# Performance work log

Hardware: AMD Instinct MI355X
Metric: run time of the kernel (lower is better)

Reference implementation:

```python
import jax, jax.numpy as jnp
import numpy as np
import math

B, T, NX, H, D = 4, 1024, 1024, 16, 64
KMAX = 32          # rel_kmax
RELV = 64          # rel_vocab_size (tree relation vocab)
NLOC = 64          # local-relation table size
SQRT = 2.0         # args.sqrt
INF = 10000000000.0


def setup_inputs() -> dict:
    key = jax.random.key(0)
    ks = jax.random.split(key, 13)
    return {
        'x': jax.random.normal(ks[0], (B, T, NX), jnp.float32),
        'rel': jax.random.randint(ks[1], (B, T, T), 0, RELV),
        'tds': jax.random.normal(ks[2], (B, H, T, T), jnp.float32) * 0.1,
        'LR_Q': jax.random.normal(ks[3], (H, NLOC, D), jnp.float32) * 0.02,
        'LR_K': jax.random.normal(ks[4], (H, NLOC, D), jnp.float32) * 0.02,
        'LR_map': jax.random.randint(ks[5], (B, T, T), 0, NLOC),
        'c_attn_w': jax.random.normal(ks[6], (NX, 3 * NX), jnp.float32) * 0.02,
        'c_attn_b': jnp.zeros((3 * NX,), jnp.float32),
        'c_proj_w': jax.random.normal(ks[7], (NX, NX), jnp.float32) * 0.02,
        'c_proj_b': jnp.zeros((NX,), jnp.float32),
        'rel_w_emb': 1.0 + jax.random.normal(ks[8], (RELV, H), jnp.float32) * 0.02,
        'rel_k_emb': jax.random.normal(ks[9], (2 * KMAX + 1, D), jnp.float32) * 0.02,
        'rel_v_emb': jax.random.normal(ks[10], (2 * KMAX + 1, D), jnp.float32) * 0.02,
    }


def reference(x, rel, tds, LR_Q, LR_K, LR_map,
              c_attn_w, c_attn_b, c_proj_w, c_proj_b,
              rel_w_emb, rel_k_emb, rel_v_emb):
    inv_sqrt_d = 1.0 / math.sqrt(D)
    # qkv projection
    qkv = x @ c_attn_w + c_attn_b                       # [B,T,3*NX]
    q, k, v = jnp.split(qkv, 3, axis=-1)
    split = lambda t: t.reshape(B, T, H, D).transpose(0, 2, 1, 3)  # [B,H,T,D]
    q, k, v = split(q), split(k), split(v)

    # relative position ids (buffer): clamp(j - i, -kmax, kmax) + kmax
    idx = jnp.arange(T)
    rel_ids = jnp.clip(idx[None, :] - idx[:, None], -KMAX, KMAX) + KMAX  # [T,T]

    # raw scores + relative-key term (use_seq)
    w = jnp.einsum('bhtd,bhsd->bhts', q, k)
    w = w + jnp.einsum('bhtd,tsd->bhts', q, rel_k_emb[rel_ids])
    w = w * inv_sqrt_d                                   # scale=True

    # multiplicative tree-relation bias (use_tree, additive=False)
    mask = jnp.tril(jnp.ones((T, T), jnp.float32))       # causal bias buffer
    relb = rel_w_emb[rel].transpose(0, 3, 1, 2)          # [B,H,T,T]
    w = w * (relb * mask)

    # top-down tree positional encoding bias
    w = w + tds

    # local-relation terms (gathered score biases)
    lr_map = jnp.broadcast_to(LR_map[:, None], (B, H, T, T))
    lr1 = jnp.einsum('bhtd,hnd->bhtn', q, LR_K) * inv_sqrt_d   # [B,H,T,NLOC]
    lr1 = jnp.take_along_axis(lr1, lr_map, axis=-1)            # [B,H,T,T]
    lr2 = jnp.einsum('hnd,bhsd->bhns', LR_Q, k) * inv_sqrt_d   # [B,H,NLOC,T]
    lr2 = jnp.take_along_axis(lr2, lr_map, axis=-2)            # [B,H,T,T]
    w = (w + lr1 + lr2) / math.sqrt(SQRT)

    # causal mask + softmax
    w = w * mask - INF * (1.0 - mask)
    p = jax.nn.softmax(w, axis=-1)

    # attention output + relative-value term
    out = jnp.einsum('bhts,bhsd->bhtd', p, v)
    out = out + jnp.einsum('bhts,tsd->bhtd', p, rel_v_emb[rel_ids])

    out = out.transpose(0, 2, 1, 3).reshape(B, T, NX)    # merge heads
    return out @ c_proj_w + c_proj_b
```

## Files before the change

### kernel.cpp

```cpp
#include <hip/hip_runtime.h>

typedef __attribute__((ext_vector_type(8))) short short8;
typedef __attribute__((ext_vector_type(4))) float fx4;

__device__ __forceinline__ unsigned short f32_to_bf16_rne(float f){
  unsigned int u = __float_as_uint(f);
  u += 0x7fffu + ((u >> 16) & 1u);
  return (unsigned short)(u >> 16);
}

__global__ void cvt_bf16(const float* __restrict__ in, unsigned short* __restrict__ out, int n4){
  int i = blockIdx.x * blockDim.x + threadIdx.x;
  if (i < n4){
    float4 v = ((const float4*)in)[i];
    ushort4 o;
    o.x = f32_to_bf16_rne(v.x); o.y = f32_to_bf16_rne(v.y);
    o.z = f32_to_bf16_rne(v.z); o.w = f32_to_bf16_rne(v.w);
    ((ushort4*)out)[i] = o;
  }
}

__global__ void transpose_cvt(const float* __restrict__ in, unsigned short* __restrict__ out,
                              int R, int C){
  __shared__ float tile[32][33];
  int c0 = blockIdx.x * 32, r0 = blockIdx.y * 32;
  int lc = threadIdx.x & 31, lr = threadIdx.x >> 5;
  #pragma unroll
  for (int i = 0; i < 32; i += 8)
    tile[lr + i][lc] = in[(size_t)(r0 + lr + i) * C + c0 + lc];
  __syncthreads();
  #pragma unroll
  for (int i = 0; i < 32; i += 8)
    out[(size_t)(c0 + lr + i) * R + r0 + lc] = f32_to_bf16_rne(tile[lc][lr + i]);
}

template<int MODE>
__global__ __launch_bounds__(256) void gemm_bf16(const unsigned short* __restrict__ A,
    const unsigned short* __restrict__ BT, const float* __restrict__ bias,
    float* __restrict__ out, int M, int N, int K)
{
  __shared__ unsigned short a_s[2][128 * 32];
  __shared__ unsigned short b_s[2][128 * 32];
  const int tid = threadIdx.x;
  const int brow = blockIdx.x * 128, bcol = blockIdx.y * 128;
  const int lane = tid & 63;
  const int wave = tid >> 6;
  const int wm = (wave >> 1) * 64, wn = (wave & 1) * 64;
  const int lanr = lane & 15, laneq = lane >> 4;

  fx4 acc[4][4];
  const fx4 zero = {0.f, 0.f, 0.f, 0.f};
  #pragma unroll
  for (int m = 0; m < 4; m++)
    #pragma unroll
    for (int n = 0; n < 4; n++) acc[m][n] = zero;

  short8 ra[2], rb[2];
  auto gload = [&](int k0){
    #pragma unroll
    for (int i = 0; i < 2; i++){
      int cc = tid + (i << 8);
      int row = cc >> 2, seg = (cc & 3) << 3;
      ra[i] = *(const short8*)(A  + (size_t)(brow + row) * K + k0 + seg);
      rb[i] = *(const short8*)(BT + (size_t)(bcol + row) * K + k0 + seg);
    }
  };
  auto lwrite = [&](int bufi){
    #pragma unroll
    for (int i = 0; i < 2; i++){
      int cc = tid + (i << 8);
      *(short8*)&a_s[bufi][cc * 8] = ra[i];
      *(short8*)&b_s[bufi][cc * 8] = rb[i];
    }
  };

  gload(0); lwrite(0); __syncthreads();
  const int NT = K / 32;
  int buf = 0;
  for (int t = 0; t < NT; t++){
    if (t + 1 < NT) gload((t + 1) * 32);
    short8 af[4], bfr[4];
    #pragma unroll
    for (int m = 0; m < 4; m++)
      af[m] = *(short8*)&a_s[buf][(wm + m * 16 + lanr) * 32 + laneq * 8];
    #pragma unroll
    for (int n = 0; n < 4; n++)
      bfr[n] = *(short8*)&b_s[buf][(wn + n * 16 + lanr) * 32 + laneq * 8];
    #pragma unroll
    for (int m = 0; m < 4; m++)
      #pragma unroll
      for (int n = 0; n < 4; n++)
        acc[m][n] = __builtin_amdgcn_mfma_f32_16x16x32_bf16(af[m], bfr[n], acc[m][n], 0, 0, 0);
    __syncthreads();
    if (t + 1 < NT){ lwrite(buf ^ 1); __syncthreads(); }
    buf ^= 1;
  }

  #pragma unroll
  for (int m = 0; m < 4; m++){
    #pragma unroll
    for (int n = 0; n < 4; n++){
      const int col = bcol + wn + n * 16 + lanr;
      const float bv = bias[col];
      #pragma unroll
      for (int r = 0; r < 4; r++){
        const int row = brow + wm + m * 16 + laneq * 4 + r;
        const float val = acc[m][n][r] + bv;
        if constexpr (MODE == 0){
          out[(size_t)row * N + col] = val;
        } else {
          const int which = col >> 10, cc2 = col & 1023;
          const int hh = cc2 >> 6, dd = cc2 & 63;
          const int bb = row >> 10, tt2 = row & 1023;
          out[((((size_t)which * 4 + bb) * 16 + hh) * 1024 + tt2) * 64 + dd] = val;
        }
      }
    }
  }
}

__global__ __launch_bounds__(64) void lr2_kernel(const float* __restrict__ LRQ,
    const float* __restrict__ kg, float* __restrict__ lr2g)
{
  __shared__ float ks[64][68];
  __shared__ float lq[16][68];
  const int lane = threadIdx.x;
  const int s0 = blockIdx.x << 6;
  const int ngrp = blockIdx.y;
  const int bh = blockIdx.z;
  const int h = bh & 15;
  for (int r = 0; r < 64; r++)
    ks[r][lane] = kg[((size_t)(bh * 1024 + s0 + r)) * 64 + lane];
  for (int r = 0; r < 16; r++)
    lq[r][lane] = LRQ[((size_t)(h * 64 + (ngrp << 4) + r)) * 64 + lane];
  __syncthreads();
  float4 kr[16];
  #pragma unroll
  for (int j = 0; j < 16; j++) kr[j] = *(float4*)&ks[lane][j << 2];
  #pragma unroll
  for (int n = 0; n < 16; n++){
    float a = 0.f;
    #pragma unroll
    for (int j = 0; j < 16; j++){
      float4 l4 = *(float4*)&lq[n][j << 2];
      a += l4.x * kr[j].x + l4.y * kr[j].y + l4.z * kr[j].z + l4.w * kr[j].w;
    }
    lr2g[((size_t)(bh * 64 + (ngrp << 4) + n)) * 1024 + s0 + lane] = a * 0.125f;
  }
}

__global__ __launch_bounds__(256, 1) void attn_kernel(
    const float* __restrict__ qg, const float* __restrict__ kg, const float* __restrict__ vg,
    const int* __restrict__ rel, const float* __restrict__ tds,
    const float* __restrict__ relw, const int* __restrict__ lrmap,
    const float* __restrict__ LRK, const float* __restrict__ lr2g,
    const float* __restrict__ rke, const float* __restrict__ rve,
    unsigned short* __restrict__ yb)
{
  __shared__ float p_s[16][1028];
  __shared__ float kv_s[128][68];
  __shared__ float lr2_s[64][132];
  __shared__ float q_s[16][68];
  __shared__ float lr1_s[16][64];
  __shared__ float qrk_s[16][36];
  __shared__ float rv_s[33][68];
  __shared__ float relw_s[64];
  __shared__ float S_s[16];

  const int tid = threadIdx.x;
  const int bid = blockIdx.x;
  const int h = bid & 15;
  const int tmp = bid >> 4;
  const int tt = tmp & 63;
  const int b = tmp >> 6;
  const int t0 = tt << 4;
  const int bh = (b << 4) + h;
  const int lane = tid & 63;
  const int wave = tid >> 6;

  if (tid < 64) relw_s[tid] = relw[tid * 16 + h];
  {
    int i = tid >> 4, d0 = (tid & 15) << 2;
    *(float4*)&q_s[i][d0] = *(const float4*)&qg[((size_t)(bh * 1024 + t0 + i)) * 64 + d0];
  }
  for (int c = tid; c < 33 * 16; c += 256){
    int r = c >> 4, d0 = (c & 15) << 2;
    *(float4*)&rv_s[r][d0] = *(const float4*)&rve[r * 64 + d0];
  }
  for (int c = tid; c < 64 * 16; c += 256){
    int r = c >> 4, d0 = (c & 15) << 2;
    *(float4*)&kv_s[r][d0] = *(const float4*)&LRK[((size_t)(h * 64 + r)) * 64 + d0];
  }
  __syncthreads();

  {
    int i = tid >> 4, n0 = (tid & 15) << 2;
    float a0 = 0, a1 = 0, a2 = 0, a3 = 0;
    #pragma unroll
    for (int d = 0; d < 64; d += 4){
      float4 qv = *(float4*)&q_s[i][d];
      float4 x0 = *(float4*)&kv_s[n0 + 0][d];
      float4 x1 = *(float4*)&kv_s[n0 + 1][d];
      float4 x2 = *(float4*)&kv_s[n0 + 2][d];
      float4 x3 = *(float4*)&kv_s[n0 + 3][d];
      a0 += qv.x * x0.x + qv.y * x0.y + qv.z * x0.z + qv.w * x0.w;
      a1 += qv.x * x1.x + qv.y * x1.y + qv.z * x1.z + qv.w * x1.w;
      a2 += qv.x * x2.x + qv.y * x2.y + qv.z * x2.z + qv.w * x2.w;
      a3 += qv.x * x3.x + qv.y * x3.y + qv.z * x3.z + qv.w * x3.w;
    }
    lr1_s[i][n0 + 0] = a0 * 0.125f;
    lr1_s[i][n0 + 1] = a1 * 0.125f;
    lr1_s[i][n0 + 2] = a2 * 0.125f;
    lr1_s[i][n0 + 3] = a3 * 0.125f;
  }
  {
    int i = tid >> 4;
    for (int r = tid & 15; r < 33; r += 16){
      float a = 0.f;
      #pragma unroll
      for (int d = 0; d < 64; d += 4){
        float4 qv = *(float4*)&q_s[i][d];
        float4 rk = *(const float4*)&rke[r * 64 + d];
        a += qv.x * rk.x + qv.y * rk.y + qv.z * rk.z + qv.w * rk.w;
      }
      qrk_s[i][r] = a;
    }
  }

  const int tmax = t0 + 15;
  const int cmax = tmax >> 7;
  const int sl = tid & 127;
  const int thalf = tid >> 7;

  for (int c = 0; c <= cmax; c++){
    const int s0 = c << 7;
    __syncthreads();
    for (int x = tid; x < 128 * 16; x += 256){
      int r = x >> 4, d0 = (x & 15) << 2;
      *(float4*)&kv_s[r][d0] = *(const float4*)&kg[((size_t)(bh * 1024 + s0 + r)) * 64 + d0];
    }
    for (int x = tid; x < 64 * 32; x += 256){
      int r = x >> 5, c4 = (x & 31) << 2;
      *(float4*)&lr2_s[r][c4] = *(const float4*)&lr2g[((size_t)(bh * 64 + r)) * 1024 + s0 + c4];
    }
    __syncthreads();
    const int sg = s0 + sl;
    float4 kr[16];
    #pragma unroll
    for (int j = 0; j < 16; j++) kr[j] = *(float4*)&kv_s[sl][j << 2];
    #pragma unroll
    for (int ti = 0; ti < 8; ti++){
      const int r = (thalf << 3) + ti;
      const int gt = t0 + r;
      const int diff = gt - sg;
      if (diff < 0){ p_s[r][sg] = -1e30f; continue; }
      float acc = 0.f;
      #pragma unroll
      for (int j = 0; j < 16; j++){
        float4 qv = *(float4*)&q_s[r][j << 2];
        acc += qv.x * kr[j].x + qv.y * kr[j].y + qv.z * kr[j].z + qv.w * kr[j].w;
      }
      const int rid = (diff < 32) ? (32 - diff) : 0;
      float logit = (acc + qrk_s[r][rid]) * 0.125f;
      const size_t pidx = ((size_t)(b * 1024 + gt)) * 1024 + sg;
      const int rl = rel[pidx];
      const int mm = lrmap[pidx];
      const float td = tds[((size_t)(bh * 1024 + gt)) * 1024 + sg];
      logit = logit * relw_s[rl] + td + lr1_s[r][mm] + lr2_s[mm][sl];
      p_s[r][sg] = logit * 0.70710678118654752f;
    }
  }
  __syncthreads();

  const int slim = (cmax + 1) << 7;
  #pragma unroll
  for (int rr = 0; rr < 4; rr++){
    const int r = (wave << 2) + rr;
    float mx = -3e38f;
    for (int s = lane; s < slim; s += 64) mx = fmaxf(mx, p_s[r][s]);
    #pragma unroll
    for (int off = 32; off; off >>= 1) mx = fmaxf(mx, __shfl_xor(mx, off));
    float sum = 0.f;
    for (int s = lane; s < slim; s += 64){
      float e = __expf(p_s[r][s] - mx);
      p_s[r][s] = e;
      sum += e;
    }
    #pragma unroll
    for (int off = 32; off; off >>= 1) sum += __shfl_xor(sum, off);
    if (lane == 0) S_s[r] = sum;
  }

  const int trow = tid >> 4;
  const int dgrp = tid & 15;
  const int gt2 = t0 + trow;
  float o0 = 0, o1 = 0, o2 = 0, o3 = 0;
  for (int c = 0; c <= cmax; c++){
    const int s0 = c << 7;
    __syncthreads();
    for (int x = tid; x < 128 * 16; x += 256){
      int r = x >> 4, d0 = (x & 15) << 2;
      *(float4*)&kv_s[r][d0] = *(const float4*)&vg[((size_t)(bh * 1024 + s0 + r)) * 64 + d0];
    }
    __syncthreads();
    const float* prow = &p_s[trow][s0];
    #pragma unroll 8
    for (int s = 0; s < 128; s++){
      float pv = prow[s];
      float4 v4 = *(float4*)&kv_s[s][dgrp << 2];
      o0 += pv * v4.x; o1 += pv * v4.y; o2 += pv * v4.z; o3 += pv * v4.w;
    }
  }

  float psum = 0.f, r0a = 0, r1a = 0, r2a = 0, r3a = 0;
  #pragma unroll
  for (int rr = 1; rr <= 32; rr++){
    int s = gt2 - 32 + rr;
    if (s >= 0){
      float pv = p_s[trow][s];
      psum += pv;
      float4 r4 = *(float4*)&rv_s[rr][dgrp << 2];
      r0a += pv * r4.x; r1a += pv * r4.y; r2a += pv * r4.z; r3a += pv * r4.w;
    }
  }
  const float S = S_s[trow];
  float pr0 = S - psum; pr0 = pr0 > 0.f ? pr0 : 0.f;
  float4 rz = *(float4*)&rv_s[0][dgrp << 2];
  r0a += pr0 * rz.x; r1a += pr0 * rz.y; r2a += pr0 * rz.z; r3a += pr0 * rz.w;
  const float inv = 1.0f / S;
  o0 = (o0 + r0a) * inv; o1 = (o1 + r1a) * inv; o2 = (o2 + r2a) * inv; o3 = (o3 + r3a) * inv;
  ushort4 ob;
  ob.x = f32_to_bf16_rne(o0); ob.y = f32_to_bf16_rne(o1);
  ob.z = f32_to_bf16_rne(o2); ob.w = f32_to_bf16_rne(o3);
  *(ushort4*)&yb[((size_t)(b * 1024 + gt2)) * 1024 + (h << 6) + (dgrp << 2)] = ob;
}

extern "C" void kernel_launch(void* const* d_in, const int* in_sizes, int n_in,
                              void* d_out, int out_size, void* d_ws, size_t ws_size,
                              hipStream_t stream)
{
  const float* x    = (const float*)d_in[0];
  const int*   rel  = (const int*)d_in[1];
  const float* tds  = (const float*)d_in[2];
  const float* LRQ  = (const float*)d_in[3];
  const float* LRK  = (const float*)d_in[4];
  const int*   lrmap= (const int*)d_in[5];
  const float* caw  = (const float*)d_in[6];
  const float* cab  = (const float*)d_in[7];
  const float* cpw  = (const float*)d_in[8];
  const float* cpb  = (const float*)d_in[9];
  const float* relw = (const float*)d_in[10];
  const float* rke  = (const float*)d_in[11];
  const float* rve  = (const float*)d_in[12];
  float* out = (float*)d_out;

  char* ws = (char*)d_ws;
  unsigned short* xb  = (unsigned short*)(ws);
  unsigned short* waT = (unsigned short*)(ws + ((size_t)8  << 20));
  unsigned short* wpT = (unsigned short*)(ws + ((size_t)14 << 20));
  float* qkv          = (float*)(ws + ((size_t)16 << 20));
  float* lr2          = (float*)(ws + ((size_t)64 << 20));
  unsigned short* yb  = (unsigned short*)(ws + ((size_t)80 << 20));

  const size_t BHTD = (size_t)4 * 16 * 1024 * 64;
  const float* qptr = qkv;
  const float* kptr = qkv + BHTD;
  const float* vptr = qkv + 2 * BHTD;

  cvt_bf16<<<4096, 256, 0, stream>>>(x, xb, 4096 * 1024 / 4);
  transpose_cvt<<<dim3(3072 / 32, 1024 / 32), 256, 0, stream>>>(caw, waT, 1024, 3072);
  transpose_cvt<<<dim3(1024 / 32, 1024 / 32), 256, 0, stream>>>(cpw, wpT, 1024, 1024);
  gemm_bf16<1><<<dim3(32, 24), 256, 0, stream>>>(xb, waT, cab, qkv, 4096, 3072, 1024);
  lr2_kernel<<<dim3(16, 4, 64), 64, 0, stream>>>(LRQ, kptr, lr2);
  attn_kernel<<<4096, 256, 0, stream>>>(qptr, kptr, vptr, rel, tds, relw, lrmap,
                                        LRK, lr2, rke, rve, yb);
  gemm_bf16<0><<<dim3(32, 8), 256, 0, stream>>>(yb, wpT, cpb, out, 4096, 1024, 1024);
}
```

Baseline: 1.338 ms.

## Rewrite attention as streaming online softmax with small LDS footprint and heavy-first order

```diff
diff --git a/kernel.cpp b/kernel.cpp
--- a/kernel.cpp
+++ b/kernel.cpp
@@ -119,37 +119,42 @@
   }
 }
 
-__global__ __launch_bounds__(64) void lr2_kernel(const float* __restrict__ LRQ,
+__global__ __launch_bounds__(256) void lr2_kernel(const float* __restrict__ LRQ,
     const float* __restrict__ kg, float* __restrict__ lr2g)
 {
-  __shared__ float ks[64][68];
-  __shared__ float lq[16][68];
-  const int lane = threadIdx.x;
-  const int s0 = blockIdx.x << 6;
-  const int ngrp = blockIdx.y;
-  const int bh = blockIdx.z;
+  __shared__ float lqT[64][68];
+  __shared__ float k_s[64][68];
+  const int tid = threadIdx.x;
+  const int bh = blockIdx.x >> 4;
+  const int s0 = (blockIdx.x & 15) << 6;
   const int h = bh & 15;
-  for (int r = 0; r < 64; r++)
-    ks[r][lane] = kg[((size_t)(bh * 1024 + s0 + r)) * 64 + lane];
-  for (int r = 0; r < 16; r++)
-    lq[r][lane] = LRQ[((size_t)(h * 64 + (ngrp << 4) + r)) * 64 + lane];
+  #pragma unroll
+  for (int p = 0; p < 4; p++){
+    int x = (p << 8) + tid;
+    int r = x >> 4, d4 = (x & 15) << 2;
+    float4 v = *(const float4*)&LRQ[((size_t)((h << 6) + r) << 6) + d4];
+    lqT[d4 + 0][r] = v.x; lqT[d4 + 1][r] = v.y; lqT[d4 + 2][r] = v.z; lqT[d4 + 3][r] = v.w;
+    *(float4*)&k_s[r][d4] = *(const float4*)&kg[((size_t)((bh << 10) + s0 + r) << 6) + d4];
+  }
   __syncthreads();
-  float4 kr[16];
-  #pragma unroll
-  for (int j = 0; j < 16; j++) kr[j] = *(float4*)&ks[lane][j << 2];
-  #pragma unroll
-  for (int n = 0; n < 16; n++){
+  const int n = tid & 63, w = tid >> 6;
+  float lqr[64];
+  #pragma unroll
+  for (int d = 0; d < 64; d++) lqr[d] = lqT[d][n];
+  #pragma unroll
+  for (int i = 0; i < 16; i++){
+    const int s = (w << 4) + i;
     float a = 0.f;
     #pragma unroll
     for (int j = 0; j < 16; j++){
-      float4 l4 = *(float4*)&lq[n][j << 2];
-      a += l4.x * kr[j].x + l4.y * kr[j].y + l4.z * kr[j].z + l4.w * kr[j].w;
-    }
-    lr2g[((size_t)(bh * 64 + (ngrp << 4) + n)) * 1024 + s0 + lane] = a * 0.125f;
-  }
-}
-
-__global__ __launch_bounds__(256, 1) void attn_kernel(
+      float4 k4 = *(float4*)&k_s[s][j << 2];
+      a += lqr[4*j]*k4.x + lqr[4*j+1]*k4.y + lqr[4*j+2]*k4.z + lqr[4*j+3]*k4.w;
+    }
+    lr2g[((size_t)((bh << 10) + s0 + s) << 6) + n] = a * 0.125f;
+  }
+}
+
+__global__ __launch_bounds__(256, 3) void attn_kernel(
     const float* __restrict__ qg, const float* __restrict__ kg, const float* __restrict__ vg,
     const int* __restrict__ rel, const float* __restrict__ tds,
     const float* __restrict__ relw, const int* __restrict__ lrmap,
@@ -157,182 +162,177 @@
     const float* __restrict__ rke, const float* __restrict__ rve,
     unsigned short* __restrict__ yb)
 {
-  __shared__ float p_s[16][1028];
-  __shared__ float kv_s[128][68];
-  __shared__ float lr2_s[64][132];
-  __shared__ float q_s[16][68];
+  __shared__ float k_s[64][64];
+  __shared__ float lr2_s[64][68];
+  __shared__ float p_s[16][64];
+  __shared__ float q_s[16][64];
   __shared__ float lr1_s[16][64];
   __shared__ float qrk_s[16][36];
-  __shared__ float rv_s[33][68];
   __shared__ float relw_s[64];
+  __shared__ float scale_s[16];
   __shared__ float S_s[16];
 
   const int tid = threadIdx.x;
   const int bid = blockIdx.x;
   const int h = bid & 15;
-  const int tmp = bid >> 4;
-  const int tt = tmp & 63;
-  const int b = tmp >> 6;
+  const int rest = bid >> 4;
+  const int b = rest & 3;
+  const int tt = 63 - (rest >> 2);
   const int t0 = tt << 4;
   const int bh = (b << 4) + h;
   const int lane = tid & 63;
   const int wave = tid >> 6;
 
   if (tid < 64) relw_s[tid] = relw[tid * 16 + h];
-  {
-    int i = tid >> 4, d0 = (tid & 15) << 2;
-    *(float4*)&q_s[i][d0] = *(const float4*)&qg[((size_t)(bh * 1024 + t0 + i)) * 64 + d0];
-  }
-  for (int c = tid; c < 33 * 16; c += 256){
-    int r = c >> 4, d0 = (c & 15) << 2;
-    *(float4*)&rv_s[r][d0] = *(const float4*)&rve[r * 64 + d0];
-  }
-  for (int c = tid; c < 64 * 16; c += 256){
-    int r = c >> 4, d0 = (c & 15) << 2;
-    *(float4*)&kv_s[r][d0] = *(const float4*)&LRK[((size_t)(h * 64 + r)) * 64 + d0];
+  { int i = tid >> 4, d4 = (tid & 15) << 2;
+    *(float4*)&q_s[i][d4] = *(const float4*)&qg[((size_t)((bh << 10) + t0 + i) << 6) + d4]; }
+  #pragma unroll
+  for (int p = 0; p < 4; p++){
+    int x = (p << 8) + tid;
+    int row = x >> 4, j = x & 15;
+    *(float4*)&k_s[row][(j ^ (row & 15)) << 2] =
+      *(const float4*)&LRK[((size_t)((h << 6) + row) << 6) + (j << 2)];
   }
   __syncthreads();
 
-  {
-    int i = tid >> 4, n0 = (tid & 15) << 2;
+  { int i = tid >> 4, n0 = (tid & 15) << 2;
     float a0 = 0, a1 = 0, a2 = 0, a3 = 0;
     #pragma unroll
-    for (int d = 0; d < 64; d += 4){
-      float4 qv = *(float4*)&q_s[i][d];
-      float4 x0 = *(float4*)&kv_s[n0 + 0][d];
-      float4 x1 = *(float4*)&kv_s[n0 + 1][d];
-      float4 x2 = *(float4*)&kv_s[n0 + 2][d];
-      float4 x3 = *(float4*)&kv_s[n0 + 3][d];
-      a0 += qv.x * x0.x + qv.y * x0.y + qv.z * x0.z + qv.w * x0.w;
-      a1 += qv.x * x1.x + qv.y * x1.y + qv.z * x1.z + qv.w * x1.w;
-      a2 += qv.x * x2.x + qv.y * x2.y + qv.z * x2.z + qv.w * x2.w;
-      a3 += qv.x * x3.x + qv.y * x3.y + qv.z * x3.z + qv.w * x3.w;
+    for (int j = 0; j < 16; j++){
+      float4 qv = *(float4*)&q_s[i][j << 2];
+      float4 x0 = *(float4*)&k_s[n0 + 0][(j ^ ((n0 + 0) & 15)) << 2];
+      float4 x1 = *(float4*)&k_s[n0 + 1][(j ^ ((n0 + 1) & 15)) << 2];
+      float4 x2 = *(float4*)&k_s[n0 + 2][(j ^ ((n0 + 2) & 15)) << 2];
+      float4 x3 = *(float4*)&k_s[n0 + 3][(j ^ ((n0 + 3) & 15)) << 2];
+      a0 += qv.x*x0.x + qv.y*x0.y + qv.z*x0.z + qv.w*x0.w;
+      a1 += qv.x*x1.x + qv.y*x1.y + qv.z*x1.z + qv.w*x1.w;
+      a2 += qv.x*x2.x + qv.y*x2.y + qv.z*x2.z + qv.w*x2.w;
+      a3 += qv.x*x3.x + qv.y*x3.y + qv.z*x3.z + qv.w*x3.w;
     }
     lr1_s[i][n0 + 0] = a0 * 0.125f;
     lr1_s[i][n0 + 1] = a1 * 0.125f;
     lr1_s[i][n0 + 2] = a2 * 0.125f;
     lr1_s[i][n0 + 3] = a3 * 0.125f;
   }
-  {
-    int i = tid >> 4;
+  { int i = tid >> 4;
     for (int r = tid & 15; r < 33; r += 16){
       float a = 0.f;
       #pragma unroll
-      for (int d = 0; d < 64; d += 4){
-        float4 qv = *(float4*)&q_s[i][d];
-        float4 rk = *(const float4*)&rke[r * 64 + d];
-        a += qv.x * rk.x + qv.y * rk.y + qv.z * rk.z + qv.w * rk.w;
+      for (int j = 0; j < 16; j++){
+        float4 qv = *(float4*)&q_s[i][j << 2];
+        float4 rk = *(const float4*)&rke[(r << 6) + (j << 2)];
+        a += qv.x*rk.x + qv.y*rk.y + qv.z*rk.z + qv.w*rk.w;
       }
       qrk_s[i][r] = a;
     }
   }
 
-  const int tmax = t0 + 15;
-  const int cmax = tmax >> 7;
-  const int sl = tid & 127;
-  const int thalf = tid >> 7;
+  float m_reg[4], S_reg[4];
+  #pragma unroll
+  for (int j = 0; j < 4; j++){ m_reg[j] = -1e30f; S_reg[j] = 0.f; }
+  const int trow = tid >> 4, dgrp = tid & 15;
+  const int gt2 = t0 + trow;
+  float o0 = 0, o1 = 0, o2 = 0, o3 = 0;
+  float ra0 = 0, ra1 = 0, ra2 = 0, ra3 = 0, ptail = 0;
+  const int sl = lane;
+  const int cmax = (t0 + 15) >> 6;
 
   for (int c = 0; c <= cmax; c++){
-    const int s0 = c << 7;
+    const int s0 = c << 6;
     __syncthreads();
-    for (int x = tid; x < 128 * 16; x += 256){
-      int r = x >> 4, d0 = (x & 15) << 2;
-      *(float4*)&kv_s[r][d0] = *(const float4*)&kg[((size_t)(bh * 1024 + s0 + r)) * 64 + d0];
-    }
-    for (int x = tid; x < 64 * 32; x += 256){
-      int r = x >> 5, c4 = (x & 31) << 2;
-      *(float4*)&lr2_s[r][c4] = *(const float4*)&lr2g[((size_t)(bh * 64 + r)) * 1024 + s0 + c4];
+    #pragma unroll
+    for (int p = 0; p < 4; p++){
+      int x = (p << 8) + tid;
+      int row = x >> 4, j = x & 15;
+      *(float4*)&k_s[row][(j ^ (row & 15)) << 2] =
+        *(const float4*)&kg[((size_t)((bh << 10) + s0 + row) << 6) + (j << 2)];
+      *(float4*)&lr2_s[row][j << 2] =
+        *(const float4*)&lr2g[((size_t)((bh << 10) + s0 + row) << 6) + (j << 2)];
     }
     __syncthreads();
+
+    float4 kr[16];
+    #pragma unroll
+    for (int j = 0; j < 16; j++) kr[j] = *(float4*)&k_s[sl][(j ^ (sl & 15)) << 2];
     const int sg = s0 + sl;
-    float4 kr[16];
-    #pragma unroll
-    for (int j = 0; j < 16; j++) kr[j] = *(float4*)&kv_s[sl][j << 2];
-    #pragma unroll
-    for (int ti = 0; ti < 8; ti++){
-      const int r = (thalf << 3) + ti;
+    #pragma unroll
+    for (int jj = 0; jj < 4; jj++){
+      const int r = (wave << 2) + jj;
       const int gt = t0 + r;
       const int diff = gt - sg;
-      if (diff < 0){ p_s[r][sg] = -1e30f; continue; }
-      float acc = 0.f;
-      #pragma unroll
-      for (int j = 0; j < 16; j++){
-        float4 qv = *(float4*)&q_s[r][j << 2];
-        acc += qv.x * kr[j].x + qv.y * kr[j].y + qv.z * kr[j].z + qv.w * kr[j].w;
-      }
-      const int rid = (diff < 32) ? (32 - diff) : 0;
-      float logit = (acc + qrk_s[r][rid]) * 0.125f;
-      const size_t pidx = ((size_t)(b * 1024 + gt)) * 1024 + sg;
-      const int rl = rel[pidx];
-      const int mm = lrmap[pidx];
-      const float td = tds[((size_t)(bh * 1024 + gt)) * 1024 + sg];
-      logit = logit * relw_s[rl] + td + lr1_s[r][mm] + lr2_s[mm][sl];
-      p_s[r][sg] = logit * 0.70710678118654752f;
-    }
+      float sc = -1e30f;
+      if (diff >= 0){
+        float acc = 0.f;
+        #pragma unroll
+        for (int j = 0; j < 16; j++){
+          float4 qv = *(float4*)&q_s[r][j << 2];
+          acc += qv.x*kr[j].x + qv.y*kr[j].y + qv.z*kr[j].z + qv.w*kr[j].w;
+        }
+        const int rid = (diff < 32) ? (32 - diff) : 0;
+        float logit = (acc + qrk_s[r][rid]) * 0.125f;
+        const size_t pidx = (((size_t)(b << 10) + gt) << 10) + sg;
+        const int rl = rel[pidx];
+        const int mm = lrmap[pidx];
+        const float td = tds[(((size_t)(bh << 10) + gt) << 10) + sg];
+        logit = logit * relw_s[rl] + td + lr1_s[r][mm] + lr2_s[sl][mm];
+        sc = logit * 0.70710678118654752f;
+      }
+      float mx = sc;
+      #pragma unroll
+      for (int off = 32; off; off >>= 1) mx = fmaxf(mx, __shfl_xor(mx, off));
+      const float mn = fmaxf(m_reg[jj], mx);
+      const float pv = (diff >= 0) ? __expf(sc - mn) : 0.f;
+      float sum = pv;
+      #pragma unroll
+      for (int off = 32; off; off >>= 1) sum += __shfl_xor(sum, off);
+      const float scl = __expf(m_reg[jj] - mn);
+      S_reg[jj] = S_reg[jj] * scl + sum;
+      m_reg[jj] = mn;
+      p_s[r][sl] = pv;
+      if (lane == 0) scale_s[r] = scl;
+    }
+    __syncthreads();
+
+    const float os = scale_s[trow];
+    o0 *= os; o1 *= os; o2 *= os; o3 *= os;
+    ra0 *= os; ra1 *= os; ra2 *= os; ra3 *= os; ptail *= os;
+    if (s0 <= gt2){
+      const float* vbase = &vg[((size_t)((bh << 10) + s0)) << 6];
+      const int smax = min(63, gt2 - s0);
+      for (int s = 0; s <= smax; s++){
+        const float pv = p_s[trow][s];
+        float4 v4 = *(const float4*)&vbase[(s << 6) + (dgrp << 2)];
+        o0 += pv*v4.x; o1 += pv*v4.y; o2 += pv*v4.z; o3 += pv*v4.w;
+      }
+      const int lo = max(s0, gt2 - 31);
+      const int hi = min(s0 + 63, gt2);
+      for (int s = lo; s <= hi; s++){
+        const float pv = p_s[trow][s - s0];
+        ptail += pv;
+        float4 r4 = *(const float4*)&rve[((s - gt2 + 32) << 6) + (dgrp << 2)];
+        ra0 += pv*r4.x; ra1 += pv*r4.y; ra2 += pv*r4.z; ra3 += pv*r4.w;
+      }
+    }
+  }
+
+  if (lane == 0){
+    #pragma unroll
+    for (int j = 0; j < 4; j++) S_s[(wave << 2) + j] = S_reg[j];
   }
   __syncthreads();
 
-  const int slim = (cmax + 1) << 7;
-  #pragma unroll
-  for (int rr = 0; rr < 4; rr++){
-    const int r = (wave << 2) + rr;
-    float mx = -3e38f;
-    for (int s = lane; s < slim; s += 64) mx = fmaxf(mx, p_s[r][s]);
-    #pragma unroll
-    for (int off = 32; off; off >>= 1) mx = fmaxf(mx, __shfl_xor(mx, off));
-    float sum = 0.f;
-    for (int s = lane; s < slim; s += 64){
-      float e = __expf(p_s[r][s] - mx);
-      p_s[r][s] = e;
-      sum += e;
-    }
-    #pragma unroll
-    for (int off = 32; off; off >>= 1) sum += __shfl_xor(sum, off);
-    if (lane == 0) S_s[r] = sum;
-  }
-
-  const int trow = tid >> 4;
-  const int dgrp = tid & 15;
-  const int gt2 = t0 + trow;
-  float o0 = 0, o1 = 0, o2 = 0, o3 = 0;
-  for (int c = 0; c <= cmax; c++){
-    const int s0 = c << 7;
-    __syncthreads();
-    for (int x = tid; x < 128 * 16; x += 256){
-      int r = x >> 4, d0 = (x & 15) << 2;
-      *(float4*)&kv_s[r][d0] = *(const float4*)&vg[((size_t)(bh * 1024 + s0 + r)) * 64 + d0];
-    }
-    __syncthreads();
-    const float* prow = &p_s[trow][s0];
-    #pragma unroll 8
-    for (int s = 0; s < 128; s++){
-      float pv = prow[s];
-      float4 v4 = *(float4*)&kv_s[s][dgrp << 2];
-      o0 += pv * v4.x; o1 += pv * v4.y; o2 += pv * v4.z; o3 += pv * v4.w;
-    }
-  }
-
-  float psum = 0.f, r0a = 0, r1a = 0, r2a = 0, r3a = 0;
-  #pragma unroll
-  for (int rr = 1; rr <= 32; rr++){
-    int s = gt2 - 32 + rr;
-    if (s >= 0){
-      float pv = p_s[trow][s];
-      psum += pv;
-      float4 r4 = *(float4*)&rv_s[rr][dgrp << 2];
-      r0a += pv * r4.x; r1a += pv * r4.y; r2a += pv * r4.z; r3a += pv * r4.w;
-    }
-  }
   const float S = S_s[trow];
-  float pr0 = S - psum; pr0 = pr0 > 0.f ? pr0 : 0.f;
-  float4 rz = *(float4*)&rv_s[0][dgrp << 2];
-  r0a += pr0 * rz.x; r1a += pr0 * rz.y; r2a += pr0 * rz.z; r3a += pr0 * rz.w;
+  float pr0 = S - ptail; pr0 = fmaxf(pr0, 0.f);
+  float4 rz = *(const float4*)&rve[dgrp << 2];
   const float inv = 1.0f / S;
-  o0 = (o0 + r0a) * inv; o1 = (o1 + r1a) * inv; o2 = (o2 + r2a) * inv; o3 = (o3 + r3a) * inv;
+  o0 = (o0 + ra0 + pr0 * rz.x) * inv;
+  o1 = (o1 + ra1 + pr0 * rz.y) * inv;
+  o2 = (o2 + ra2 + pr0 * rz.z) * inv;
+  o3 = (o3 + ra3 + pr0 * rz.w) * inv;
   ushort4 ob;
   ob.x = f32_to_bf16_rne(o0); ob.y = f32_to_bf16_rne(o1);
   ob.z = f32_to_bf16_rne(o2); ob.w = f32_to_bf16_rne(o3);
-  *(ushort4*)&yb[((size_t)(b * 1024 + gt2)) * 1024 + (h << 6) + (dgrp << 2)] = ob;
+  *(ushort4*)&yb[((size_t)((b << 10) + gt2) << 10) + (h << 6) + (dgrp << 2)] = ob;
 }
 
 extern "C" void kernel_launch(void* const* d_in, const int* in_sizes, int n_in,
@@ -371,7 +371,7 @@
   transpose_cvt<<<dim3(3072 / 32, 1024 / 32), 256, 0, stream>>>(caw, waT, 1024, 3072);
   transpose_cvt<<<dim3(1024 / 32, 1024 / 32), 256, 0, stream>>>(cpw, wpT, 1024, 1024);
   gemm_bf16<1><<<dim3(32, 24), 256, 0, stream>>>(xb, waT, cab, qkv, 4096, 3072, 1024);
-  lr2_kernel<<<dim3(16, 4, 64), 64, 0, stream>>>(LRQ, kptr, lr2);
+  lr2_kernel<<<dim3(1024), 256, 0, stream>>>(LRQ, kptr, lr2);
   attn_kernel<<<4096, 256, 0, stream>>>(qptr, kptr, vptr, rel, tds, relw, lrmap,
                                         LRK, lr2, rke, rve, yb);
   gemm_bf16<0><<<dim3(32, 8), 256, 0, stream>>>(yb, wpT, cpb, out, 4096, 1024, 1024);
```

New measurement: 1.118 ms. 1.2x faster.
